# Kernel optimization log

Hardware: AMD Instinct MI355X
Metric: run time of the kernel (lower is better)

Reference implementation:

```python
import jax, jax.numpy as jnp
from jax import lax
import numpy as np

N = 32768; K = 8; M = 8192; G = 32; EF = 128

def _lrelu(x):
    return jnp.where(x > 0, x, 0.01 * x)

def _pc_res(x, W1, b1, W2, b2):
    h = _lrelu(x @ W1 + b1) @ W2 + b2
    return _lrelu(h + x)

def _conv3d(x, w, b):
    dn = ('NCDHW', 'OIDHW', 'NCDHW')
    return lax.conv_general_dilated(x, w, (1, 1, 1), 'SAME', dimension_numbers=dn) + b[None, :, None, None, None]

def setup_inputs():
    key = jax.random.key(0)
    ks = jax.random.split(key, 32)
    f32 = jnp.float32
    pc_KNN_idx = jax.random.randint(ks[0], (N * K,), 0, N, dtype=jnp.int32)
    pc_KNN_xyz = jax.random.normal(ks[1], (N * K, 3), dtype=f32)
    flat = jax.random.permutation(ks[2], G * G * G)[:M]  # unique voxel coords -> deterministic scatter
    voxel_xyz_int = jnp.stack([flat // (G * G), (flat // G) % G, flat % G], axis=1).astype(jnp.int32)
    voxel_KNN_idx = jax.random.randint(ks[3], (M * K,), 0, N, dtype=jnp.int32)
    voxel_KNN_xyz = jax.random.normal(ks[4], (M * K, 3), dtype=f32)
    s = 0.05
    def rn(i, shape):
        return jax.random.normal(ks[i], shape, dtype=f32) * s
    return dict(
        pc_KNN_idx=pc_KNN_idx, pc_KNN_xyz=pc_KNN_xyz, voxel_xyz_int=voxel_xyz_int,
        voxel_KNN_idx=voxel_KNN_idx, voxel_KNN_xyz=voxel_KNN_xyz,
        pcf_W1=rn(5, (3, EF)), pcf_b1=rn(6, (EF,)), pcf_W2=rn(7, (EF, EF)), pcf_b2=rn(8, (EF,)),
        pcres_W1=rn(9, (7, EF, EF)), pcres_b1=rn(10, (7, EF)),
        pcres_W2=rn(11, (7, EF, EF)), pcres_b2=rn(12, (7, EF)),
        pcc_W1=rn(13, (6, EF + 3, EF)), pcc_b1=rn(14, (6, EF)),
        pcc_W2=rn(15, (6, EF, EF)), pcc_b2=rn(16, (6, EF)),
        r3_Wc1=rn(17, (8, EF, EF, 3, 3, 3)), r3_bc1=rn(18, (8, EF)),
        r3_Wc2=rn(19, (8, EF, EF, 1, 1, 1)), r3_bc2=rn(20, (8, EF)),
        lin1_W=rn(21, (EF, EF)), lin1_b=rn(22, (EF,)),
        lin2_W=rn(23, (EF, EF)), lin2_b=rn(24, (EF,)),
        linb_W=rn(25, (EF, 3)), linb_b=rn(26, (3,)),
    )

def reference(pc_KNN_idx, pc_KNN_xyz, voxel_xyz_int, voxel_KNN_idx, voxel_KNN_xyz,
              pcf_W1, pcf_b1, pcf_W2, pcf_b2,
              pcres_W1, pcres_b1, pcres_W2, pcres_b2,
              pcc_W1, pcc_b1, pcc_W2, pcc_b2,
              r3_Wc1, r3_bc1, r3_Wc2, r3_bc2,
              lin1_W, lin1_b, lin2_W, lin2_b, linb_W, linb_b):
    # pc_conv_first: MLP on KNN relative xyz, max-pool over K neighbors -> [N, EF]
    out = _lrelu(pc_KNN_xyz @ pcf_W1 + pcf_b1) @ pcf_W2 + pcf_b2
    out = jnp.max(out.reshape(-1, K, EF), axis=1)
    out = _lrelu(out)
    out = _pc_res(out, pcres_W1[0], pcres_b1[0], pcres_W2[0], pcres_b2[0])
    for i in range(6):
        idx = pc_KNN_idx if i < 5 else voxel_KNN_idx
        xyz = pc_KNN_xyz if i < 5 else voxel_KNN_xyz
        g = jnp.concatenate([out[idx], xyz], axis=1)            # [R*K, EF+3]
        h = _lrelu(g @ pcc_W1[i] + pcc_b1[i]) @ pcc_W2[i] + pcc_b2[i]
        out = _lrelu(jnp.max(h.reshape(-1, K, EF), axis=1))     # [R, EF]
        out = _pc_res(out, pcres_W1[i + 1], pcres_b1[i + 1], pcres_W2[i + 1], pcres_b2[i + 1])
    # scatter voxel features into a dense grid (coords are unique)
    vi = voxel_xyz_int - jnp.min(voxel_xyz_int, axis=0)
    grid = jnp.zeros((G, G, G, EF), jnp.float32).at[vi[:, 0], vi[:, 1], vi[:, 2]].set(out)
    x = grid.transpose(3, 0, 1, 2)[None]                        # [1, EF, G, G, G]
    for i in range(8):
        y = _lrelu(_conv3d(x, r3_Wc1[i], r3_bc1[i]))
        y = _conv3d(y, r3_Wc2[i], r3_bc2[i])
        x = _lrelu(y + x)
    out = x[0].transpose(1, 2, 3, 0)[vi[:, 0], vi[:, 1], vi[:, 2]]  # gather back [M, EF]
    out = _lrelu(out @ lin1_W + lin1_b)
    out = _lrelu(out @ lin2_W + lin2_b)
    return jax.nn.sigmoid(out @ linb_W + linb_b)                # out_bool head [M, 3]
```

## Files before the change

kernel.cpp:

```cpp
#include <hip/hip_runtime.h>
#include <math.h>

#define EF 128
#define NPTS 32768
#define KNN 8
#define MVOX 8192
#define GDIM 32
#define NVOXG (GDIM*GDIM*GDIM)

typedef __attribute__((ext_vector_type(8))) short bfrag;
typedef __attribute__((ext_vector_type(4))) float f32x4;

__device__ __forceinline__ float lrelu(float x) { return x > 0.f ? x : 0.01f * x; }
__device__ __forceinline__ short f2b(float f) {
    unsigned u = __float_as_uint(f);
    return (short)((u + 0x7fff + ((u >> 16) & 1)) >> 16);
}
#define MFMA(a,b,c) __builtin_amdgcn_mfma_f32_16x16x32_bf16((a),(b),(c),0,0,0)
__device__ __forceinline__ int swz(int row, int bytecol) {
    return row * 256 + (bytecol ^ ((row & 7) << 4));
}

__global__ void k_pack_w(const float* __restrict__ src, short* __restrict__ dst,
                         int K_real, int n_steps, int k_str, int c_str) {
    int t = blockIdx.x * 256 + threadIdx.x;
    int total = n_steps * 4096;
    if (t >= total) return;
    int r = t & 7, l = (t >> 3) & 63, ct = (t >> 9) & 7, s = t >> 12;
    int k = s * 32 + (l >> 4) * 8 + r;
    int col = ct * 16 + (l & 15);
    float v = (k < K_real) ? src[(size_t)k * k_str + (size_t)col * c_str] : 0.f;
    dst[t] = f2b(v);
}
__global__ void k_pack_wc1(const float* __restrict__ src, short* __restrict__ dst) {
    int t = blockIdx.x * 256 + threadIdx.x;
    if (t >= 108 * 4096) return;
    int r = t & 7, l = (t >> 3) & 63, ct = (t >> 9) & 7, s = t >> 12;
    int tap = s >> 2;
    int ci = (s & 3) * 32 + (l >> 4) * 8 + r;
    int col = ct * 16 + (l & 15);
    dst[t] = f2b(src[((size_t)col * 128 + ci) * 27 + tap]);
}


__global__ __launch_bounds__(512) void k_pcfirst(
    const float* __restrict__ xyz, const short* __restrict__ w1p, const float* __restrict__ b1,
    const short* __restrict__ w2p, const float* __restrict__ b2,
    const short* __restrict__ rw1p, const float* __restrict__ rb1,
    const short* __restrict__ rw2p, const float* __restrict__ rb2,
    float* __restrict__ out32, short* __restrict__ out16) {
    __shared__ __align__(16) char tb[32768];
    int wid = threadIdx.x >> 6, lane = threadIdx.x & 63, lrow = lane & 15, lq = lane >> 4;
    int wm = wid >> 2, wn = wid & 3;
    int rowbase = blockIdx.x * 128;
    f32x4 zv = {0.f, 0.f, 0.f, 0.f};
    {
        f32x4 acc1[4][2];
        #pragma unroll
        for (int rt = 0; rt < 4; ++rt) { acc1[rt][0] = zv; acc1[rt][1] = zv; }
        bfrag Bv[2];
        #pragma unroll
        for (int ct = 0; ct < 2; ++ct) Bv[ct] = ((const bfrag*)w1p)[(wn * 2 + ct) * 64 + lane];
        #pragma unroll
        for (int rt = 0; rt < 4; ++rt) {
            bfrag a4;
            #pragma unroll
            for (int r = 0; r < 8; ++r) a4[r] = 0;
            if (lq == 0) {
                int gr = rowbase + wm * 64 + rt * 16 + lrow;
                a4[0] = f2b(xyz[gr * 3]); a4[1] = f2b(xyz[gr * 3 + 1]); a4[2] = f2b(xyz[gr * 3 + 2]);
            }
            #pragma unroll
            for (int ct = 0; ct < 2; ++ct) acc1[rt][ct] = MFMA(a4, Bv[ct], acc1[rt][ct]);
        }
        float bb1[2];
        #pragma unroll
        for (int ct = 0; ct < 2; ++ct) bb1[ct] = b1[wn * 32 + ct * 16 + lrow];
        #pragma unroll
        for (int rt = 0; rt < 4; ++rt)
            #pragma unroll
            for (int ct = 0; ct < 2; ++ct)
                #pragma unroll
                for (int r = 0; r < 4; ++r) {
                    int row = wm * 64 + rt * 16 + lq * 4 + r, col = wn * 32 + ct * 16 + lrow;
                    *(short*)(tb + swz(row, col * 2)) = f2b(lrelu(acc1[rt][ct][r] + bb1[ct]));
                }
    }
    __syncthreads();
    float bb2[2];
    #pragma unroll
    for (int ct = 0; ct < 2; ++ct) bb2[ct] = b2[wn * 32 + ct * 16 + lrow];
    f32x4 acc[4][2];
    #pragma unroll
    for (int rt = 0; rt < 4; ++rt) { acc[rt][0] = zv; acc[rt][1] = zv; }
    const bfrag* bp2 = (const bfrag*)w2p;
    #pragma unroll
    for (int s = 0; s < 4; ++s) {
        bfrag Bv[2];
        #pragma unroll
        for (int ct = 0; ct < 2; ++ct) Bv[ct] = bp2[(s * 8 + wn * 2 + ct) * 64 + lane];
        bfrag av[4];
        #pragma unroll
        for (int rt = 0; rt < 4; ++rt) {
            int row = wm * 64 + rt * 16 + lrow;
            av[rt] = *(const bfrag*)(tb + swz(row, s * 64 + lq * 16));
        }
        #pragma unroll
        for (int ct = 0; ct < 2; ++ct)
            #pragma unroll
            for (int rt = 0; rt < 4; ++rt) acc[rt][ct] = MFMA(av[rt], Bv[ct], acc[rt][ct]);
    }
    float pv[4][2];
    #pragma unroll
    for (int rt = 0; rt < 4; ++rt)
        #pragma unroll
        for (int ct = 0; ct < 2; ++ct) {
            float m = -INFINITY;
            #pragma unroll
            for (int r = 0; r < 4; ++r) m = fmaxf(m, acc[rt][ct][r] + bb2[ct]);
            m = fmaxf(m, __shfl_xor(m, 16, 64));
            pv[rt][ct] = lrelu(m);
        }
    __syncthreads();
    float* xf = (float*)(tb + 4096);
    char*  tres = tb + 12544;
    if ((lq & 1) == 0) {
        #pragma unroll
        for (int rt = 0; rt < 4; ++rt)
            #pragma unroll
            for (int ct = 0; ct < 2; ++ct) {
                int row = wm * 8 + rt * 2 + (lq >> 1), col = wn * 32 + ct * 16 + lrow;
                *(short*)(tb + swz(row, col * 2)) = f2b(pv[rt][ct]);
                xf[row * 130 + col] = pv[rt][ct];
            }
    }
    __syncthreads();
    {
        f32x4 r1 = zv;
        #pragma unroll
        for (int s = 0; s < 4; ++s) {
            bfrag B = ((const bfrag*)rw1p)[(s * 8 + wid) * 64 + lane];
            bfrag a = *(const bfrag*)(tb + swz(lrow, s * 64 + lq * 16));
            r1 = MFMA(a, B, r1);
        }
        float rb1v = rb1[wid * 16 + lrow];
        #pragma unroll
        for (int r = 0; r < 4; ++r) {
            int row = lq * 4 + r;
            *(short*)(tres + swz(row, (wid * 16 + lrow) * 2)) = f2b(lrelu(r1[r] + rb1v));
        }
    }
    __syncthreads();
    {
        f32x4 r2 = zv;
        #pragma unroll
        for (int s = 0; s < 4; ++s) {
            bfrag B = ((const bfrag*)rw2p)[(s * 8 + wid) * 64 + lane];
            bfrag a = *(const bfrag*)(tres + swz(lrow, s * 64 + lq * 16));
            r2 = MFMA(a, B, r2);
        }
        float rb2v = rb2[wid * 16 + lrow];
        int p0 = blockIdx.x * 16;
        #pragma unroll
        for (int r = 0; r < 4; ++r) {
            int row = lq * 4 + r, col = wid * 16 + lrow;
            float v = lrelu(r2[r] + rb2v + xf[row * 130 + col]);
            size_t o = (size_t)(p0 + row) * 128 + col;
            out16[o] = f2b(v);
            if (out32) out32[o] = v;
        }
    }
}

__global__ __launch_bounds__(512) void k_pcconv(
    const short* __restrict__ fin16, const int* __restrict__ idx, const float* __restrict__ xyz,
    const short* __restrict__ w1p, const float* __restrict__ b1,
    const short* __restrict__ w2p, const float* __restrict__ b2,
    const short* __restrict__ rw1p, const float* __restrict__ rb1,
    const short* __restrict__ rw2p, const float* __restrict__ rb2,
    float* __restrict__ out32, short* __restrict__ out16) {
    __shared__ __align__(16) char tb[32768];
    int wid = threadIdx.x >> 6, lane = threadIdx.x & 63, lrow = lane & 15, lq = lane >> 4;
    int wm = wid >> 2, wn = wid & 3;
    int rowbase = blockIdx.x * 128;
    f32x4 zv = {0.f, 0.f, 0.f, 0.f};
    {
        int srow = threadIdx.x >> 2, sseg = threadIdx.x & 3;
        int nb = idx[rowbase + srow];
        const bfrag* src = (const bfrag*)(fin16 + (size_t)nb * 128);
        #pragma unroll
        for (int j = 0; j < 4; ++j) {
            int seg = sseg + j * 4;
            bfrag v = src[seg];
            *(bfrag*)(tb + swz(srow, seg * 16)) = v;
        }
    }
    __syncthreads();
    float bb1[2], bb2[2];
    #pragma unroll
    for (int ct = 0; ct < 2; ++ct) {
        bb1[ct] = b1[wn * 32 + ct * 16 + lrow];
        bb2[ct] = b2[wn * 32 + ct * 16 + lrow];
    }
    f32x4 acc[4][2];
    #pragma unroll
    for (int rt = 0; rt < 4; ++rt) { acc[rt][0] = zv; acc[rt][1] = zv; }
    const bfrag* bp1 = (const bfrag*)w1p;
    #pragma unroll
    for (int s = 0; s < 4; ++s) {
        bfrag Bv[2];
        #pragma unroll
        for (int ct = 0; ct < 2; ++ct) Bv[ct] = bp1[(s * 8 + wn * 2 + ct) * 64 + lane];
        bfrag av[4];
        #pragma unroll
        for (int rt = 0; rt < 4; ++rt) {
            int row = wm * 64 + rt * 16 + lrow;
            av[rt] = *(const bfrag*)(tb + swz(row, s * 64 + lq * 16));
        }
        #pragma unroll
        for (int ct = 0; ct < 2; ++ct)
            #pragma unroll
            for (int rt = 0; rt < 4; ++rt) acc[rt][ct] = MFMA(av[rt], Bv[ct], acc[rt][ct]);
    }
    {
        bfrag Bv[2];
        #pragma unroll
        for (int ct = 0; ct < 2; ++ct) Bv[ct] = bp1[(32 + wn * 2 + ct) * 64 + lane];
        #pragma unroll
        for (int rt = 0; rt < 4; ++rt) {
            bfrag a4;
            #pragma unroll
            for (int r = 0; r < 8; ++r) a4[r] = 0;
            if (lq == 0) {
                int gr = rowbase + wm * 64 + rt * 16 + lrow;
                a4[0] = f2b(xyz[gr * 3]); a4[1] = f2b(xyz[gr * 3 + 1]); a4[2] = f2b(xyz[gr * 3 + 2]);
            }
            #pragma unroll
            for (int ct = 0; ct < 2; ++ct) acc[rt][ct] = MFMA(a4, Bv[ct], acc[rt][ct]);
        }
    }
    __syncthreads();
    #pragma unroll
    for (int rt = 0; rt < 4; ++rt)
        #pragma unroll
        for (int ct = 0; ct < 2; ++ct)
            #pragma unroll
            for (int r = 0; r < 4; ++r) {
                int row = wm * 64 + rt * 16 + lq * 4 + r, col = wn * 32 + ct * 16 + lrow;
                *(short*)(tb + swz(row, col * 2)) = f2b(lrelu(acc[rt][ct][r] + bb1[ct]));
            }
    __syncthreads();
    f32x4 acc2[4][2];
    #pragma unroll
    for (int rt = 0; rt < 4; ++rt) { acc2[rt][0] = zv; acc2[rt][1] = zv; }
    const bfrag* bp2 = (const bfrag*)w2p;
    #pragma unroll
    for (int s = 0; s < 4; ++s) {
        bfrag Bv[2];
        #pragma unroll
        for (int ct = 0; ct < 2; ++ct) Bv[ct] = bp2[(s * 8 + wn * 2 + ct) * 64 + lane];
        bfrag av[4];
        #pragma unroll
        for (int rt = 0; rt < 4; ++rt) {
            int row = wm * 64 + rt * 16 + lrow;
            av[rt] = *(const bfrag*)(tb + swz(row, s * 64 + lq * 16));
        }
        #pragma unroll
        for (int ct = 0; ct < 2; ++ct)
            #pragma unroll
            for (int rt = 0; rt < 4; ++rt) acc2[rt][ct] = MFMA(av[rt], Bv[ct], acc2[rt][ct]);
    }
    float pv[4][2];
    #pragma unroll
    for (int rt = 0; rt < 4; ++rt)
        #pragma unroll
        for (int ct = 0; ct < 2; ++ct) {
            float m = -INFINITY;
            #pragma unroll
            for (int r = 0; r < 4; ++r) m = fmaxf(m, acc2[rt][ct][r] + bb2[ct]);
            m = fmaxf(m, __shfl_xor(m, 16, 64));
            pv[rt][ct] = lrelu(m);
        }
    __syncthreads();
    float* xf = (float*)(tb + 4096);
    char*  tres = tb + 12544;
    if ((lq & 1) == 0) {
        #pragma unroll
        for (int rt = 0; rt < 4; ++rt)
            #pragma unroll
            for (int ct = 0; ct < 2; ++ct) {
                int row = wm * 8 + rt * 2 + (lq >> 1), col = wn * 32 + ct * 16 + lrow;
                *(short*)(tb + swz(row, col * 2)) = f2b(pv[rt][ct]);
                xf[row * 130 + col] = pv[rt][ct];
            }
    }
    __syncthreads();
    {
        f32x4 r1 = zv;
        #pragma unroll
        for (int s = 0; s < 4; ++s) {
            bfrag B = ((const bfrag*)rw1p)[(s * 8 + wid) * 64 + lane];
            bfrag a = *(const bfrag*)(tb + swz(lrow, s * 64 + lq * 16));
            r1 = MFMA(a, B, r1);
        }
        float rb1v = rb1[wid * 16 + lrow];
        #pragma unroll
        for (int r = 0; r < 4; ++r) {
            int row = lq * 4 + r;
            *(short*)(tres + swz(row, (wid * 16 + lrow) * 2)) = f2b(lrelu(r1[r] + rb1v));
        }
    }
    __syncthreads();
    {
        f32x4 r2 = zv;
        #pragma unroll
        for (int s = 0; s < 4; ++s) {
            bfrag B = ((const bfrag*)rw2p)[(s * 8 + wid) * 64 + lane];
            bfrag a = *(const bfrag*)(tres + swz(lrow, s * 64 + lq * 16));
            r2 = MFMA(a, B, r2);
        }
        float rb2v = rb2[wid * 16 + lrow];
        int p0 = blockIdx.x * 16;
        #pragma unroll
        for (int r = 0; r < 4; ++r) {
            int row = lq * 4 + r, col = wid * 16 + lrow;
            float v = lrelu(r2[r] + rb2v + xf[row * 130 + col]);
            size_t o = (size_t)(p0 + row) * 128 + col;
            out16[o] = f2b(v);
            if (out32) out32[o] = v;
        }
    }
}

__global__ __launch_bounds__(512) void k_conv3(
    const float* __restrict__ gin32, const short* __restrict__ gin16,
    const short* __restrict__ w1p, const float* __restrict__ b1,
    const short* __restrict__ w2p, const float* __restrict__ b2,
    float* __restrict__ gout32, short* __restrict__ gout16) {
    __shared__ __align__(16) char Ab[2][32768];
    int wid = threadIdx.x >> 6, lane = threadIdx.x & 63, lrow = lane & 15, lq = lane >> 4;
    int wm = wid >> 2, wn = wid & 3;
    int va = blockIdx.x >> 3, vb0 = (blockIdx.x & 7) * 4;
    int srow = threadIdx.x >> 2, sseg = threadIdx.x & 3;
    int sb = srow >> 5, sc = srow & 31;
    bfrag zf;
    #pragma unroll
    for (int r = 0; r < 8; ++r) zf[r] = 0;
    float bb1[2], bb2[2];
    #pragma unroll
    for (int ct = 0; ct < 2; ++ct) {
        bb1[ct] = b1[wn * 32 + ct * 16 + lrow];
        bb2[ct] = b2[wn * 32 + ct * 16 + lrow];
    }
    f32x4 zv = {0.f, 0.f, 0.f, 0.f};
    f32x4 acc[4][2];
    #pragma unroll
    for (int rt = 0; rt < 4; ++rt) { acc[rt][0] = zv; acc[rt][1] = zv; }
    const bfrag* bp1 = (const bfrag*)w1p;

    bfrag Bcur[8];
    #pragma unroll
    for (int s = 0; s < 4; ++s)
        #pragma unroll
        for (int ct = 0; ct < 2; ++ct) Bcur[s * 2 + ct] = bp1[(s * 8 + wn * 2 + ct) * 64 + lane];
    {
        int aa = va - 1, bb = vb0 + sb - 1, cc = sc - 1;
        bool ok = ((unsigned)aa < 32u) && ((unsigned)bb < 32u) && ((unsigned)cc < 32u);
        int soff = ok ? ((aa * 32 + bb) * 32 + cc) * 128 : 0;
        const bfrag* src = (const bfrag*)(gin16 + soff);
        #pragma unroll
        for (int j = 0; j < 4; ++j) {
            int seg = sseg + j * 4;
            bfrag v = src[seg];
            *(bfrag*)(Ab[0] + swz(srow, seg * 16)) = ok ? v : zf;
        }
    }
    __syncthreads();

    #pragma unroll 1
    for (int tap = 0; tap < 27; ++tap) {
        bfrag st[4];
        bool okn = false;
        bfrag Bnxt[8];
        if (tap < 26) {
            int tn = tap + 1;
            int da = tn / 9 - 1, db = (tn / 3) % 3 - 1, dc = tn % 3 - 1;
            int aa = va + da, bb = vb0 + sb + db, cc = sc + dc;
            okn = ((unsigned)aa < 32u) && ((unsigned)bb < 32u) && ((unsigned)cc < 32u);
            int soff = okn ? ((aa * 32 + bb) * 32 + cc) * 128 : 0;
            const bfrag* src = (const bfrag*)(gin16 + soff);
            #pragma unroll
            for (int j = 0; j < 4; ++j) st[j] = src[sseg + j * 4];
            #pragma unroll
            for (int s = 0; s < 4; ++s)
                #pragma unroll
                for (int ct = 0; ct < 2; ++ct)
                    Bnxt[s * 2 + ct] = bp1[((tn * 4 + s) * 8 + wn * 2 + ct) * 64 + lane];
        }
        const char* tbc = Ab[tap & 1];
        #pragma unroll
        for (int s = 0; s < 4; ++s) {
            bfrag av[4];
            #pragma unroll
            for (int rt = 0; rt < 4; ++rt) {
                int row = wm * 64 + rt * 16 + lrow;
                av[rt] = *(const bfrag*)(tbc + swz(row, s * 64 + lq * 16));
            }
            #pragma unroll
            for (int ct = 0; ct < 2; ++ct)
                #pragma unroll
                for (int rt = 0; rt < 4; ++rt) acc[rt][ct] = MFMA(av[rt], Bcur[s * 2 + ct], acc[rt][ct]);
        }
        if (tap < 26) {
            char* nb = Ab[(tap + 1) & 1];
            #pragma unroll
            for (int j = 0; j < 4; ++j)
                *(bfrag*)(nb + swz(srow, (sseg + j * 4) * 16)) = okn ? st[j] : zf;
            #pragma unroll
            for (int i = 0; i < 8; ++i) Bcur[i] = Bnxt[i];
        }
        __syncthreads();
    }

    #pragma unroll
    for (int rt = 0; rt < 4; ++rt)
        #pragma unroll
        for (int ct = 0; ct < 2; ++ct)
            #pragma unroll
            for (int r = 0; r < 4; ++r) {
                int row = wm * 64 + rt * 16 + lq * 4 + r, col = wn * 32 + ct * 16 + lrow;
                *(short*)(Ab[0] + swz(row, col * 2)) = f2b(lrelu(acc[rt][ct][r] + bb1[ct]));
            }
    __syncthreads();
    f32x4 acc2[4][2];
    #pragma unroll
    for (int rt = 0; rt < 4; ++rt) { acc2[rt][0] = zv; acc2[rt][1] = zv; }
    const bfrag* bp2 = (const bfrag*)w2p;
    #pragma unroll
    for (int s = 0; s < 4; ++s) {
        bfrag Bv[2];
        #pragma unroll
        for (int ct = 0; ct < 2; ++ct) Bv[ct] = bp2[(s * 8 + wn * 2 + ct) * 64 + lane];
        bfrag av[4];
        #pragma unroll
        for (int rt = 0; rt < 4; ++rt) {
            int row = wm * 64 + rt * 16 + lrow;
            av[rt] = *(const bfrag*)(Ab[0] + swz(row, s * 64 + lq * 16));
        }
        #pragma unroll
        for (int ct = 0; ct < 2; ++ct)
            #pragma unroll
            for (int rt = 0; rt < 4; ++rt) acc2[rt][ct] = MFMA(av[rt], Bv[ct], acc2[rt][ct]);
    }
    #pragma unroll
    for (int rt = 0; rt < 4; ++rt)
        #pragma unroll
        for (int ct = 0; ct < 2; ++ct)
            #pragma unroll
            for (int r = 0; r < 4; ++r) {
                int row = wm * 64 + rt * 16 + lq * 4 + r;
                int voxel = (va * 32 + vb0 + (row >> 5)) * 32 + (row & 31);
                size_t o = (size_t)voxel * 128 + wn * 32 + ct * 16 + lrow;
                float v = lrelu(acc2[rt][ct][r] + bb2[ct] + gin32[o]);
                gout32[o] = v; gout16[o] = f2b(v);
            }
}

__global__ __launch_bounds__(512) void k_head(
    const short* __restrict__ g16, const int* __restrict__ vx, const int* __restrict__ vmin,
    const short* __restrict__ w1p, const float* __restrict__ b1,
    const short* __restrict__ w2p, const float* __restrict__ b2,
    const float* __restrict__ W3, const float* __restrict__ b3,
    float* __restrict__ out) {
    __shared__ __align__(16) char tb[16384];
    __shared__ float t2[64][129];
    int wid = threadIdx.x >> 6, lane = threadIdx.x & 63, lrow = lane & 15, lq = lane >> 4;
    int rowbase = blockIdx.x * 64;
    int goff[4];
    #pragma unroll
    for (int rt = 0; rt < 4; ++rt) {
        int m = rowbase + rt * 16 + lrow;
        int v0 = vx[m * 3 + 0] - vmin[0];
        int v1 = vx[m * 3 + 1] - vmin[1];
        int v2 = vx[m * 3 + 2] - vmin[2];
        goff[rt] = ((v0 * 32 + v1) * 32 + v2) * 128;
    }
    float bb1 = b1[wid * 16 + lrow], bb2 = b2[wid * 16 + lrow];
    f32x4 zv = {0.f, 0.f, 0.f, 0.f};
    f32x4 acc[4];
    #pragma unroll
    for (int rt = 0; rt < 4; ++rt) acc[rt] = zv;
    const bfrag* bp1 = (const bfrag*)w1p;
    #pragma unroll
    for (int s = 0; s < 4; ++s) {
        bfrag B = bp1[(s * 8 + wid) * 64 + lane];
        #pragma unroll
        for (int rt = 0; rt < 4; ++rt) {
            bfrag a = *((const bfrag*)(g16 + goff[rt]) + s * 4 + lq);
            acc[rt] = MFMA(a, B, acc[rt]);
        }
    }
    #pragma unroll
    for (int rt = 0; rt < 4; ++rt)
        #pragma unroll
        for (int r = 0; r < 4; ++r) {
            int row = rt * 16 + lq * 4 + r, col = wid * 16 + lrow;
            *(short*)(tb + swz(row, col * 2)) = f2b(lrelu(acc[rt][r] + bb1));
        }
    __syncthreads();
    f32x4 acc2[4];
    #pragma unroll
    for (int rt = 0; rt < 4; ++rt) acc2[rt] = zv;
    const bfrag* bp2 = (const bfrag*)w2p;
    #pragma unroll
    for (int s = 0; s < 4; ++s) {
        bfrag B = bp2[(s * 8 + wid) * 64 + lane];
        #pragma unroll
        for (int rt = 0; rt < 4; ++rt) {
            int row = rt * 16 + lrow;
            bfrag av = *(const bfrag*)(tb + swz(row, s * 64 + lq * 16));
            acc2[rt] = MFMA(av, B, acc2[rt]);
        }
    }
    #pragma unroll
    for (int rt = 0; rt < 4; ++rt)
        #pragma unroll
        for (int r = 0; r < 4; ++r) {
            int row = rt * 16 + lq * 4 + r, col = wid * 16 + lrow;
            t2[row][col] = lrelu(acc2[rt][r] + bb2);
        }
    __syncthreads();
    if (threadIdx.x < 192) {
        int row = threadIdx.x & 63, c = threadIdx.x >> 6;
        float s = b3[c];
        #pragma unroll 4
        for (int k = 0; k < 128; ++k) s += t2[row][k] * W3[k * 3 + c];
        out[(size_t)(rowbase + row) * 3 + c] = 1.f / (1.f + expf(-s));
    }
}

__global__ void k_vmin(const int* __restrict__ vx, int M, int* __restrict__ vmin) {
    __shared__ int sm[3 * 256];
    int t = threadIdx.x;
    int m0 = 0x7fffffff, m1 = 0x7fffffff, m2 = 0x7fffffff;
    for (int i = t; i < M; i += 256) {
        m0 = min(m0, vx[i * 3 + 0]); m1 = min(m1, vx[i * 3 + 1]); m2 = min(m2, vx[i * 3 + 2]);
    }
    sm[t] = m0; sm[256 + t] = m1; sm[512 + t] = m2;
    __syncthreads();
    for (int s = 128; s > 0; s >>= 1) {
        if (t < s) {
            sm[t] = min(sm[t], sm[t + s]);
            sm[256 + t] = min(sm[256 + t], sm[256 + t + s]);
            sm[512 + t] = min(sm[512 + t], sm[512 + t + s]);
        }
        __syncthreads();
    }
    if (t == 0) { vmin[0] = sm[0]; vmin[1] = sm[256]; vmin[2] = sm[512]; }
}

__global__ void k_scatter(const float* __restrict__ vf, const int* __restrict__ vx,
                          const int* __restrict__ vmin, float* __restrict__ g32, short* __restrict__ g16) {
    int m = blockIdx.x, j = threadIdx.x;
    int v0 = vx[m * 3 + 0] - vmin[0];
    int v1 = vx[m * 3 + 1] - vmin[1];
    int v2 = vx[m * 3 + 2] - vmin[2];
    size_t o = (size_t)(((v0 * GDIM) + v1) * GDIM + v2) * EF + j;
    float v = vf[(size_t)m * EF + j];
    g32[o] = v; g16[o] = f2b(v);
}

extern "C" void kernel_launch(void* const* d_in, const int* in_sizes, int n_in,
                              void* d_out, int out_size, void* d_ws, size_t ws_size,
                              hipStream_t stream) {
    const int*   pc_idx  = (const int*)  d_in[0];
    const float* pc_xyz  = (const float*)d_in[1];
    const int*   vox_int = (const int*)  d_in[2];
    const int*   vox_idx = (const int*)  d_in[3];
    const float* vox_xyz = (const float*)d_in[4];
    const float* pcf_W1  = (const float*)d_in[5];
    const float* pcf_b1  = (const float*)d_in[6];
    const float* pcf_W2  = (const float*)d_in[7];
    const float* pcf_b2  = (const float*)d_in[8];
    const float* pcres_W1 = (const float*)d_in[9];
    const float* pcres_b1 = (const float*)d_in[10];
    const float* pcres_W2 = (const float*)d_in[11];
    const float* pcres_b2 = (const float*)d_in[12];
    const float* pcc_W1  = (const float*)d_in[13];
    const float* pcc_b1  = (const float*)d_in[14];
    const float* pcc_W2  = (const float*)d_in[15];
    const float* pcc_b2  = (const float*)d_in[16];
    const float* r3_Wc1  = (const float*)d_in[17];
    const float* r3_bc1  = (const float*)d_in[18];
    const float* r3_Wc2  = (const float*)d_in[19];
    const float* r3_bc2  = (const float*)d_in[20];
    const float* lin1_W  = (const float*)d_in[21];
    const float* lin1_b  = (const float*)d_in[22];
    const float* lin2_W  = (const float*)d_in[23];
    const float* lin2_b  = (const float*)d_in[24];
    const float* linb_W  = (const float*)d_in[25];
    const float* linb_b  = (const float*)d_in[26];

    const size_t NE = (size_t)NPTS * EF;
    float* A32 = (float*)d_ws;
    float* B32 = A32 + NE;
    short* A16 = (short*)(B32 + NE);
    short* B16 = A16 + NE;
    float* Y32 = (float*)(B16 + NE);
    short* Y16 = (short*)(Y32 + NE);
    short* pcf_w1p = Y16 + NE;
    short* pcf_w2p = pcf_w1p + 1 * 4096;
    short* pcc_w1p = pcf_w2p + 4 * 4096;
    short* pcc_w2p = pcc_w1p + 6 * 5 * 4096;
    short* pcr_w1p = pcc_w2p + 6 * 4 * 4096;
    short* pcr_w2p = pcr_w1p + 7 * 4 * 4096;
    short* wc2p    = pcr_w2p + 7 * 4 * 4096;
    short* lin1p   = wc2p    + 8 * 4 * 4096;
    short* lin2p   = lin1p   + 4 * 4096;
    short* wc1p    = lin2p   + 4 * 4096;
    int*   vmin    = (int*)(wc1p + 108 * 4096);

    k_pack_w<<<16, 256, 0, stream>>>(pcf_W1, pcf_w1p, 3, 1, 128, 1);
    k_pack_w<<<64, 256, 0, stream>>>(pcf_W2, pcf_w2p, 128, 4, 128, 1);
    for (int i = 0; i < 6; ++i) {
        k_pack_w<<<80, 256, 0, stream>>>(pcc_W1 + (size_t)i * 131 * 128, pcc_w1p + (size_t)i * 5 * 4096, 131, 5, 128, 1);
        k_pack_w<<<64, 256, 0, stream>>>(pcc_W2 + (size_t)i * 128 * 128, pcc_w2p + (size_t)i * 4 * 4096, 128, 4, 128, 1);
    }
    for (int i = 0; i < 7; ++i) {
        k_pack_w<<<64, 256, 0, stream>>>(pcres_W1 + (size_t)i * 128 * 128, pcr_w1p + (size_t)i * 4 * 4096, 128, 4, 128, 1);
        k_pack_w<<<64, 256, 0, stream>>>(pcres_W2 + (size_t)i * 128 * 128, pcr_w2p + (size_t)i * 4 * 4096, 128, 4, 128, 1);
    }
    for (int i = 0; i < 8; ++i)
        k_pack_w<<<64, 256, 0, stream>>>(r3_Wc2 + (size_t)i * 128 * 128, wc2p + (size_t)i * 4 * 4096, 128, 4, 1, 128);
    k_pack_w<<<64, 256, 0, stream>>>(lin1_W, lin1p, 128, 4, 128, 1);
    k_pack_w<<<64, 256, 0, stream>>>(lin2_W, lin2p, 128, 4, 128, 1);

    k_pcfirst<<<NPTS * KNN / 128, 512, 0, stream>>>(pc_xyz, pcf_w1p, pcf_b1, pcf_w2p, pcf_b2,
        pcr_w1p, pcres_b1, pcr_w2p, pcres_b2, nullptr, A16);
    short* cur16 = A16; short* nxt16 = B16;
    for (int i = 0; i < 5; ++i) {
        k_pcconv<<<NPTS * KNN / 128, 512, 0, stream>>>(cur16, pc_idx, pc_xyz,
            pcc_w1p + (size_t)i * 5 * 4096, pcc_b1 + i * EF,
            pcc_w2p + (size_t)i * 4 * 4096, pcc_b2 + i * EF,
            pcr_w1p + (size_t)(i + 1) * 4 * 4096, pcres_b1 + (i + 1) * EF,
            pcr_w2p + (size_t)(i + 1) * 4 * 4096, pcres_b2 + (i + 1) * EF,
            nullptr, nxt16);
        short* t = cur16; cur16 = nxt16; nxt16 = t;
    }
    k_pcconv<<<MVOX * KNN / 128, 512, 0, stream>>>(cur16, vox_idx, vox_xyz,
        pcc_w1p + (size_t)5 * 5 * 4096, pcc_b1 + 5 * EF,
        pcc_w2p + (size_t)5 * 4 * 4096, pcc_b2 + 5 * EF,
        pcr_w1p + (size_t)6 * 4 * 4096, pcres_b1 + 6 * EF,
        pcr_w2p + (size_t)6 * 4 * 4096, pcres_b2 + 6 * EF,
        A32, A16);

    k_vmin<<<1, 256, 0, stream>>>(vox_int, MVOX, vmin);
    hipMemsetAsync(B32, 0, NE * sizeof(float), stream);
    hipMemsetAsync(B16, 0, NE * sizeof(short), stream);
    k_scatter<<<MVOX, 128, 0, stream>>>(A32, vox_int, vmin, B32, B16);

    float* cur32 = B32; short* curg = B16;
    float* nxt32 = Y32; short* nxtg = Y16;
    for (int i = 0; i < 8; ++i) {
        k_pack_wc1<<<1728, 256, 0, stream>>>(r3_Wc1 + (size_t)i * 128 * 128 * 27, wc1p);
        k_conv3<<<256, 512, 0, stream>>>(cur32, curg, wc1p, r3_bc1 + i * EF,
                                         wc2p + (size_t)i * 4 * 4096, r3_bc2 + i * EF,
                                         nxt32, nxtg);
        float* t32 = cur32; cur32 = nxt32; nxt32 = t32;
        short* t16 = curg; curg = nxtg; nxtg = t16;
    }

    k_head<<<MVOX / 64, 512, 0, stream>>>(curg, vox_int, vmin,
                                          lin1p, lin1_b, lin2p, lin2_b, linb_W, linb_b,
                                          (float*)d_out);
}
```

Before: 748.0 us.

## Reuse a haloed input slab across in-plane taps in the 3x3x3 conv kernel

The 3D conv kernel no longer reloads a shifted 128-row input tile for each of the 27 taps. It now loads one haloed slab (4 b-rows x 32 c) per depth offset, 3 loads in total, and reads the 9 in-plane taps from shared memory using row offsets, with the c-boundary handled by masking. The output tile per block shrinks to 64 voxels, so the grid doubles to 512 blocks. Weight fragments are fetched inside the tap loop rather than double-buffered in registers. This cuts global gathers and barriers, but it halves the MFMA work per weight load and exposes weight-load latency.

```diff
diff --git a/kernel.cpp b/kernel.cpp
--- a/kernel.cpp
+++ b/kernel.cpp
@@ -340,33 +340,24 @@
     __shared__ __align__(16) char Ab[2][32768];
     int wid = threadIdx.x >> 6, lane = threadIdx.x & 63, lrow = lane & 15, lq = lane >> 4;
     int wm = wid >> 2, wn = wid & 3;
-    int va = blockIdx.x >> 3, vb0 = (blockIdx.x & 7) * 4;
+    int va = blockIdx.x >> 4, vb0 = (blockIdx.x & 15) * 2;
     int srow = threadIdx.x >> 2, sseg = threadIdx.x & 3;
-    int sb = srow >> 5, sc = srow & 31;
+    int sbl = srow >> 5, sc = srow & 31;
     bfrag zf;
     #pragma unroll
     for (int r = 0; r < 8; ++r) zf[r] = 0;
-    float bb1[2], bb2[2];
-    #pragma unroll
-    for (int ct = 0; ct < 2; ++ct) {
-        bb1[ct] = b1[wn * 32 + ct * 16 + lrow];
-        bb2[ct] = b2[wn * 32 + ct * 16 + lrow];
-    }
     f32x4 zv = {0.f, 0.f, 0.f, 0.f};
-    f32x4 acc[4][2];
-    #pragma unroll
-    for (int rt = 0; rt < 4; ++rt) { acc[rt][0] = zv; acc[rt][1] = zv; }
+    f32x4 acc[2][2];
+    #pragma unroll
+    for (int rt = 0; rt < 2; ++rt) { acc[rt][0] = zv; acc[rt][1] = zv; }
     const bfrag* bp1 = (const bfrag*)w1p;
 
-    bfrag Bcur[8];
-    #pragma unroll
-    for (int s = 0; s < 4; ++s)
-        #pragma unroll
-        for (int ct = 0; ct < 2; ++ct) Bcur[s * 2 + ct] = bp1[(s * 8 + wn * 2 + ct) * 64 + lane];
-    {
-        int aa = va - 1, bb = vb0 + sb - 1, cc = sc - 1;
-        bool ok = ((unsigned)aa < 32u) && ((unsigned)bb < 32u) && ((unsigned)cc < 32u);
-        int soff = ok ? ((aa * 32 + bb) * 32 + cc) * 128 : 0;
+    int sb = vb0 - 1 + sbl;
+    bool okb = (unsigned)sb < 32u;
+    {
+        int aa = va - 1;
+        bool ok = okb && ((unsigned)aa < 32u);
+        size_t soff = ok ? (size_t)((aa * 32 + sb) * 32 + sc) * 128 : 0;
         const bfrag* src = (const bfrag*)(gin16 + soff);
         #pragma unroll
         for (int j = 0; j < 4; ++j) {
@@ -378,88 +369,100 @@
     __syncthreads();
 
     #pragma unroll 1
-    for (int tap = 0; tap < 27; ++tap) {
+    for (int dai = 0; dai < 3; ++dai) {
         bfrag st[4];
         bool okn = false;
-        bfrag Bnxt[8];
-        if (tap < 26) {
-            int tn = tap + 1;
-            int da = tn / 9 - 1, db = (tn / 3) % 3 - 1, dc = tn % 3 - 1;
-            int aa = va + da, bb = vb0 + sb + db, cc = sc + dc;
-            okn = ((unsigned)aa < 32u) && ((unsigned)bb < 32u) && ((unsigned)cc < 32u);
-            int soff = okn ? ((aa * 32 + bb) * 32 + cc) * 128 : 0;
+        if (dai < 2) {
+            int aa = va + dai;
+            okn = okb && ((unsigned)aa < 32u);
+            size_t soff = okn ? (size_t)((aa * 32 + sb) * 32 + sc) * 128 : 0;
             const bfrag* src = (const bfrag*)(gin16 + soff);
             #pragma unroll
             for (int j = 0; j < 4; ++j) st[j] = src[sseg + j * 4];
-            #pragma unroll
-            for (int s = 0; s < 4; ++s)
+        }
+        const char* slab = Ab[dai & 1];
+        int tapbase = dai * 9;
+        #pragma unroll 3
+        for (int t9 = 0; t9 < 9; ++t9) {
+            int db = t9 / 3 - 1, dc = t9 % 3 - 1;
+            int tap = tapbase + t9;
+            int blr = (wm + db + 1) * 32;
+            #pragma unroll
+            for (int s = 0; s < 4; ++s) {
+                bfrag Bv[2];
                 #pragma unroll
                 for (int ct = 0; ct < 2; ++ct)
-                    Bnxt[s * 2 + ct] = bp1[((tn * 4 + s) * 8 + wn * 2 + ct) * 64 + lane];
-        }
-        const char* tbc = Ab[tap & 1];
-        #pragma unroll
-        for (int s = 0; s < 4; ++s) {
-            bfrag av[4];
-            #pragma unroll
-            for (int rt = 0; rt < 4; ++rt) {
-                int row = wm * 64 + rt * 16 + lrow;
-                av[rt] = *(const bfrag*)(tbc + swz(row, s * 64 + lq * 16));
-            }
-            #pragma unroll
-            for (int ct = 0; ct < 2; ++ct)
+                    Bv[ct] = bp1[((tap * 4 + s) * 8 + wn * 2 + ct) * 64 + lane];
+                bfrag av[2];
                 #pragma unroll
-                for (int rt = 0; rt < 4; ++rt) acc[rt][ct] = MFMA(av[rt], Bcur[s * 2 + ct], acc[rt][ct]);
-        }
-        if (tap < 26) {
-            char* nb = Ab[(tap + 1) & 1];
+                for (int rt = 0; rt < 2; ++rt) {
+                    int ci = rt * 16 + lrow + dc;
+                    bool ok = (unsigned)ci < 32u;
+                    int sl = blr + (ok ? ci : 0);
+                    bfrag t = *(const bfrag*)(slab + swz(sl, s * 64 + lq * 16));
+                    av[rt] = ok ? t : zf;
+                }
+                #pragma unroll
+                for (int ct = 0; ct < 2; ++ct)
+                    #pragma unroll
+                    for (int rt = 0; rt < 2; ++rt) acc[rt][ct] = MFMA(av[rt], Bv[ct], acc[rt][ct]);
+            }
+        }
+        if (dai < 2) {
+            char* nb = Ab[(dai + 1) & 1];
             #pragma unroll
             for (int j = 0; j < 4; ++j)
                 *(bfrag*)(nb + swz(srow, (sseg + j * 4) * 16)) = okn ? st[j] : zf;
-            #pragma unroll
-            for (int i = 0; i < 8; ++i) Bcur[i] = Bnxt[i];
         }
         __syncthreads();
     }
 
-    #pragma unroll
-    for (int rt = 0; rt < 4; ++rt)
+    float bb1[2], bb2[2];
+    #pragma unroll
+    for (int ct = 0; ct < 2; ++ct) {
+        bb1[ct] = b1[wn * 32 + ct * 16 + lrow];
+        bb2[ct] = b2[wn * 32 + ct * 16 + lrow];
+    }
+    #pragma unroll
+    for (int rt = 0; rt < 2; ++rt)
         #pragma unroll
         for (int ct = 0; ct < 2; ++ct)
             #pragma unroll
             for (int r = 0; r < 4; ++r) {
-                int row = wm * 64 + rt * 16 + lq * 4 + r, col = wn * 32 + ct * 16 + lrow;
+                int row = wm * 32 + rt * 16 + lq * 4 + r, col = wn * 32 + ct * 16 + lrow;
                 *(short*)(Ab[0] + swz(row, col * 2)) = f2b(lrelu(acc[rt][ct][r] + bb1[ct]));
             }
     __syncthreads();
-    f32x4 acc2[4][2];
-    #pragma unroll
-    for (int rt = 0; rt < 4; ++rt) { acc2[rt][0] = zv; acc2[rt][1] = zv; }
+    f32x4 acc2[2][2];
+    #pragma unroll
+    for (int rt = 0; rt < 2; ++rt) { acc2[rt][0] = zv; acc2[rt][1] = zv; }
     const bfrag* bp2 = (const bfrag*)w2p;
     #pragma unroll
     for (int s = 0; s < 4; ++s) {
         bfrag Bv[2];
         #pragma unroll
         for (int ct = 0; ct < 2; ++ct) Bv[ct] = bp2[(s * 8 + wn * 2 + ct) * 64 + lane];
-        bfrag av[4];
-        #pragma unroll
-        for (int rt = 0; rt < 4; ++rt) {
-            int row = wm * 64 + rt * 16 + lrow;
+        bfrag av[2];
+        #pragma unroll
+        for (int rt = 0; rt < 2; ++rt) {
+            int row = wm * 32 + rt * 16 + lrow;
             av[rt] = *(const bfrag*)(Ab[0] + swz(row, s * 64 + lq * 16));
         }
         #pragma unroll
         for (int ct = 0; ct < 2; ++ct)
             #pragma unroll
-            for (int rt = 0; rt < 4; ++rt) acc2[rt][ct] = MFMA(av[rt], Bv[ct], acc2[rt][ct]);
-    }
-    #pragma unroll
-    for (int rt = 0; rt < 4; ++rt)
+            for (int rt = 0; rt < 2; ++rt) acc2[rt][ct] = MFMA(av[rt], Bv[ct], acc2[rt][ct]);
+    }
+    #pragma unroll
+    for (int rt = 0; rt < 2; ++rt)
         #pragma unroll
         for (int ct = 0; ct < 2; ++ct)
             #pragma unroll
             for (int r = 0; r < 4; ++r) {
-                int row = wm * 64 + rt * 16 + lq * 4 + r;
-                int voxel = (va * 32 + vb0 + (row >> 5)) * 32 + (row & 31);
+                int row = wm * 32 + rt * 16 + lq * 4 + r;
+                int voxel = (va * 32 + vb0 + wm) * 32 + row - wm * 32 + wm * 32;
+                int c = rt * 16 + lq * 4 + r;
+                voxel = (va * 32 + vb0 + wm) * 32 + c;
                 size_t o = (size_t)voxel * 128 + wn * 32 + ct * 16 + lrow;
                 float v = lrelu(acc2[rt][ct][r] + bb2[ct] + gin32[o]);
                 gout32[o] = v; gout16[o] = f2b(v);
@@ -663,7 +666,7 @@
     float* nxt32 = Y32; short* nxtg = Y16;
     for (int i = 0; i < 8; ++i) {
         k_pack_wc1<<<1728, 256, 0, stream>>>(r3_Wc1 + (size_t)i * 128 * 128 * 27, wc1p);
-        k_conv3<<<256, 512, 0, stream>>>(cur32, curg, wc1p, r3_bc1 + i * EF,
+        k_conv3<<<512, 512, 0, stream>>>(cur32, curg, wc1p, r3_bc1 + i * EF,
                                          wc2p + (size_t)i * 4 * 4096, r3_bc2 + i * EF,
                                          nxt32, nxtg);
         float* t32 = cur32; cur32 = nxt32; nxt32 = t32;
```

Result: faster. 701.9 us (-6.2%).

## Stage haloed slab per depth plane in conv3 and split K across warp pairs

Applied to the files above, without the earlier changes.

The 3x3x3 conv kernel no longer reloads a shifted 128-row input tile from global memory for each of the 27 taps. It now loads a haloed 6x32 slab once per depth offset and serves the 9 in-plane taps from LDS by shifting row indices, with out-of-range columns masked to zero. Warps are regrouped into 2 K-groups by 2 N-groups by 2 M-groups, each warp holding a 64x64 accumulator. The two K-halves are summed through LDS before the epilogue. This trades less global and LDS staging traffic and fewer barriers for more accumulator registers, an extra cross-warp reduction, and no prefetch overlap of the next slab.

```diff
diff --git a/kernel.cpp b/kernel.cpp
--- a/kernel.cpp
+++ b/kernel.cpp
@@ -337,101 +337,105 @@
     const short* __restrict__ w1p, const float* __restrict__ b1,
     const short* __restrict__ w2p, const float* __restrict__ b2,
     float* __restrict__ gout32, short* __restrict__ gout16) {
-    __shared__ __align__(16) char Ab[2][32768];
+    __shared__ __align__(16) char Ab[65536];
     int wid = threadIdx.x >> 6, lane = threadIdx.x & 63, lrow = lane & 15, lq = lane >> 4;
-    int wm = wid >> 2, wn = wid & 3;
+    int kg = wid & 1, wn = (wid >> 1) & 1, wm = wid >> 2;
     int va = blockIdx.x >> 3, vb0 = (blockIdx.x & 7) * 4;
-    int srow = threadIdx.x >> 2, sseg = threadIdx.x & 3;
-    int sb = srow >> 5, sc = srow & 31;
     bfrag zf;
     #pragma unroll
     for (int r = 0; r < 8; ++r) zf[r] = 0;
-    float bb1[2], bb2[2];
-    #pragma unroll
-    for (int ct = 0; ct < 2; ++ct) {
-        bb1[ct] = b1[wn * 32 + ct * 16 + lrow];
-        bb2[ct] = b2[wn * 32 + ct * 16 + lrow];
-    }
     f32x4 zv = {0.f, 0.f, 0.f, 0.f};
-    f32x4 acc[4][2];
-    #pragma unroll
-    for (int rt = 0; rt < 4; ++rt) { acc[rt][0] = zv; acc[rt][1] = zv; }
+    f32x4 acc[4][4];
+    #pragma unroll
+    for (int rt = 0; rt < 4; ++rt)
+        #pragma unroll
+        for (int ct = 0; ct < 4; ++ct) acc[rt][ct] = zv;
     const bfrag* bp1 = (const bfrag*)w1p;
 
-    bfrag Bcur[8];
-    #pragma unroll
-    for (int s = 0; s < 4; ++s)
-        #pragma unroll
-        for (int ct = 0; ct < 2; ++ct) Bcur[s * 2 + ct] = bp1[(s * 8 + wn * 2 + ct) * 64 + lane];
-    {
-        int aa = va - 1, bb = vb0 + sb - 1, cc = sc - 1;
-        bool ok = ((unsigned)aa < 32u) && ((unsigned)bb < 32u) && ((unsigned)cc < 32u);
-        int soff = ok ? ((aa * 32 + bb) * 32 + cc) * 128 : 0;
-        const bfrag* src = (const bfrag*)(gin16 + soff);
-        #pragma unroll
-        for (int j = 0; j < 4; ++j) {
-            int seg = sseg + j * 4;
-            bfrag v = src[seg];
-            *(bfrag*)(Ab[0] + swz(srow, seg * 16)) = ok ? v : zf;
-        }
-    }
-    __syncthreads();
-
     #pragma unroll 1
-    for (int tap = 0; tap < 27; ++tap) {
-        bfrag st[4];
-        bool okn = false;
-        bfrag Bnxt[8];
-        if (tap < 26) {
-            int tn = tap + 1;
-            int da = tn / 9 - 1, db = (tn / 3) % 3 - 1, dc = tn % 3 - 1;
-            int aa = va + da, bb = vb0 + sb + db, cc = sc + dc;
-            okn = ((unsigned)aa < 32u) && ((unsigned)bb < 32u) && ((unsigned)cc < 32u);
-            int soff = okn ? ((aa * 32 + bb) * 32 + cc) * 128 : 0;
-            const bfrag* src = (const bfrag*)(gin16 + soff);
-            #pragma unroll
-            for (int j = 0; j < 4; ++j) st[j] = src[sseg + j * 4];
-            #pragma unroll
-            for (int s = 0; s < 4; ++s)
+    for (int dai = 0; dai < 3; ++dai) {
+        __syncthreads();
+        {
+            int aa = va + dai - 1;
+            bool aok = (unsigned)aa < 32u;
+            #pragma unroll
+            for (int j = 0; j < 6; ++j) {
+                int task = (int)threadIdx.x + j * 512;
+                int srow = task >> 4, seg = task & 15;
+                int bl = srow >> 5, c = srow & 31;
+                int sb = vb0 - 1 + bl;
+                bool ok = aok && ((unsigned)sb < 32u);
+                size_t gb = ok ? ((size_t)((aa * 32 + sb) * 32 + c) * 128 + seg * 8) : 0;
+                bfrag v = *((const bfrag*)gin16 + gb / 8);
+                *(bfrag*)(Ab + swz(srow, seg * 16)) = ok ? v : zf;
+            }
+        }
+        __syncthreads();
+        #pragma unroll
+        for (int t9 = 0; t9 < 9; ++t9) {
+            int db = t9 / 3 - 1, dc = t9 % 3 - 1;
+            int tap = dai * 9 + t9;
+            #pragma unroll
+            for (int ss = 0; ss < 2; ++ss) {
+                int s = kg * 2 + ss;
+                bfrag Bv[4];
                 #pragma unroll
-                for (int ct = 0; ct < 2; ++ct)
-                    Bnxt[s * 2 + ct] = bp1[((tn * 4 + s) * 8 + wn * 2 + ct) * 64 + lane];
-        }
-        const char* tbc = Ab[tap & 1];
-        #pragma unroll
-        for (int s = 0; s < 4; ++s) {
-            bfrag av[4];
-            #pragma unroll
-            for (int rt = 0; rt < 4; ++rt) {
-                int row = wm * 64 + rt * 16 + lrow;
-                av[rt] = *(const bfrag*)(tbc + swz(row, s * 64 + lq * 16));
-            }
-            #pragma unroll
-            for (int ct = 0; ct < 2; ++ct)
+                for (int ct = 0; ct < 4; ++ct)
+                    Bv[ct] = bp1[((tap * 4 + s) * 8 + wn * 4 + ct) * 64 + lane];
+                bfrag av[4];
                 #pragma unroll
-                for (int rt = 0; rt < 4; ++rt) acc[rt][ct] = MFMA(av[rt], Bcur[s * 2 + ct], acc[rt][ct]);
-        }
-        if (tap < 26) {
-            char* nb = Ab[(tap + 1) & 1];
-            #pragma unroll
-            for (int j = 0; j < 4; ++j)
-                *(bfrag*)(nb + swz(srow, (sseg + j * 4) * 16)) = okn ? st[j] : zf;
-            #pragma unroll
-            for (int i = 0; i < 8; ++i) Bcur[i] = Bnxt[i];
-        }
-        __syncthreads();
-    }
-
-    #pragma unroll
-    for (int rt = 0; rt < 4; ++rt)
-        #pragma unroll
-        for (int ct = 0; ct < 2; ++ct)
-            #pragma unroll
-            for (int r = 0; r < 4; ++r) {
-                int row = wm * 64 + rt * 16 + lq * 4 + r, col = wn * 32 + ct * 16 + lrow;
-                *(short*)(Ab[0] + swz(row, col * 2)) = f2b(lrelu(acc[rt][ct][r] + bb1[ct]));
-            }
-    __syncthreads();
+                for (int rt = 0; rt < 4; ++rt) {
+                    int ci = ((rt & 1) << 4) + lrow + dc;
+                    bool ok = (unsigned)ci < 32u;
+                    int srow2 = (wm * 2 + db + 1 + (rt >> 1)) * 32 + (ok ? ci : 0);
+                    bfrag t = *(const bfrag*)(Ab + swz(srow2, s * 64 + lq * 16));
+                    av[rt] = ok ? t : zf;
+                }
+                #pragma unroll
+                for (int ct = 0; ct < 4; ++ct)
+                    #pragma unroll
+                    for (int rt = 0; rt < 4; ++rt) acc[rt][ct] = MFMA(av[rt], Bv[ct], acc[rt][ct]);
+            }
+        }
+    }
+    __syncthreads();
+    if (kg == 1) {
+        int p = wm * 2 + wn;
+        #pragma unroll
+        for (int rt = 0; rt < 4; ++rt)
+            #pragma unroll
+            for (int ct = 0; ct < 4; ++ct)
+                *(f32x4*)(Ab + p * 16384 + ((rt * 4 + ct) * 64 + lane) * 16) = acc[rt][ct];
+    }
+    __syncthreads();
+    if (kg == 0) {
+        int p = wm * 2 + wn;
+        #pragma unroll
+        for (int rt = 0; rt < 4; ++rt)
+            #pragma unroll
+            for (int ct = 0; ct < 4; ++ct)
+                acc[rt][ct] += *(const f32x4*)(Ab + p * 16384 + ((rt * 4 + ct) * 64 + lane) * 16);
+    }
+    __syncthreads();
+    if (kg == 0) {
+        float bb1[4];
+        #pragma unroll
+        for (int ct = 0; ct < 4; ++ct) bb1[ct] = b1[wn * 64 + ct * 16 + lrow];
+        #pragma unroll
+        for (int rt = 0; rt < 4; ++rt)
+            #pragma unroll
+            for (int ct = 0; ct < 4; ++ct)
+                #pragma unroll
+                for (int r = 0; r < 4; ++r) {
+                    int row = wm * 64 + rt * 16 + lq * 4 + r, col = wn * 64 + ct * 16 + lrow;
+                    *(short*)(Ab + swz(row, col * 2)) = f2b(lrelu(acc[rt][ct][r] + bb1[ct]));
+                }
+    }
+    __syncthreads();
+    int wm2 = wid >> 2, wn2 = wid & 3;
+    float bb2[2];
+    #pragma unroll
+    for (int ct = 0; ct < 2; ++ct) bb2[ct] = b2[wn2 * 32 + ct * 16 + lrow];
     f32x4 acc2[4][2];
     #pragma unroll
     for (int rt = 0; rt < 4; ++rt) { acc2[rt][0] = zv; acc2[rt][1] = zv; }
@@ -440,12 +444,12 @@
     for (int s = 0; s < 4; ++s) {
         bfrag Bv[2];
         #pragma unroll
-        for (int ct = 0; ct < 2; ++ct) Bv[ct] = bp2[(s * 8 + wn * 2 + ct) * 64 + lane];
+        for (int ct = 0; ct < 2; ++ct) Bv[ct] = bp2[(s * 8 + wn2 * 2 + ct) * 64 + lane];
         bfrag av[4];
         #pragma unroll
         for (int rt = 0; rt < 4; ++rt) {
-            int row = wm * 64 + rt * 16 + lrow;
-            av[rt] = *(const bfrag*)(Ab[0] + swz(row, s * 64 + lq * 16));
+            int row = wm2 * 64 + rt * 16 + lrow;
+            av[rt] = *(const bfrag*)(Ab + swz(row, s * 64 + lq * 16));
         }
         #pragma unroll
         for (int ct = 0; ct < 2; ++ct)
@@ -458,9 +462,9 @@
         for (int ct = 0; ct < 2; ++ct)
             #pragma unroll
             for (int r = 0; r < 4; ++r) {
-                int row = wm * 64 + rt * 16 + lq * 4 + r;
+                int row = wm2 * 64 + rt * 16 + lq * 4 + r;
                 int voxel = (va * 32 + vb0 + (row >> 5)) * 32 + (row & 31);
-                size_t o = (size_t)voxel * 128 + wn * 32 + ct * 16 + lrow;
+                size_t o = (size_t)voxel * 128 + wn2 * 32 + ct * 16 + lrow;
                 float v = lrelu(acc2[rt][ct][r] + bb2[ct] + gin32[o]);
                 gout32[o] = v; gout16[o] = f2b(v);
             }
```

After: 714.4 us. 1.05x faster.
